# Kernel tuning notes

Measured on AMD Instinct MI355X. Metric: run time of the kernel, lower is better.

The kernel has to match this reference:

```python
import jax, jax.numpy as jnp
import numpy as np

VOCAB = 32
UTT_LEN = 16
NUM_MEANING_TYPES = 5
MEANINGS_PER_TYPE = 10
SUPPORT_SIZE = 100000  # = MEANINGS_PER_TYPE ** NUM_MEANING_TYPES
BATCH = 2048


def setup_inputs() -> dict:
    key = jax.random.key(0)
    k1, k2, k3 = jax.random.split(key, 3)
    # query utterances: [utt_len, batch] token ids
    utts = jax.random.randint(k1, (UTT_LEN, BATCH), 0, VOCAB, dtype=jnp.int64)
    # support set is stored as one-hot encoded utterances [S, utt_len*vocab]
    support_tokens = jax.random.randint(k2, (SUPPORT_SIZE, UTT_LEN), 0, VOCAB)
    support = jax.nn.one_hot(support_tokens, VOCAB, dtype=jnp.float32)
    support = support.reshape(SUPPORT_SIZE, UTT_LEN * VOCAB)
    # meanings table [S, num_meaning_types]
    meanings_t = jax.random.randint(k3, (SUPPORT_SIZE, NUM_MEANING_TYPES), 0,
                                    MEANINGS_PER_TYPE, dtype=jnp.int64)
    return {"utts": utts, "support": support, "meanings_t": meanings_t}


def reference(utts, support, meanings_t):
    # utts: [M, N] ints; support: [S, M*V] floats; meanings_t: [S, T] ints
    M, N = utts.shape
    # one-hot encode queries: [N, M, V] -> [N, M*V]
    batch_fluffy = jax.nn.one_hot(utts.T, VOCAB, dtype=jnp.float32).reshape(N, M * VOCAB)
    batch_sq = jnp.sum(batch_fluffy * batch_fluffy, axis=1)        # [N]
    support_sq = jnp.sum(support * support, axis=1)                # [S]
    cross = batch_fluffy @ support.T                                # [N, S]
    squared_dist = batch_sq[:, None] + support_sq[None, :] - 2.0 * cross
    # top-1 smallest distance (K=1)
    top1 = jnp.argmin(squared_dist, axis=1)                         # [N]
    meanings = meanings_t[top1]                                     # [N, T]
    return jax.nn.one_hot(meanings, MEANINGS_PER_TYPE, dtype=jnp.float32)
```

## Files before the change

kernel.cpp:

```cpp
#include <hip/hip_runtime.h>
#include <stdint.h>

#define S_ROWS 100000
#define NQ     2048
#define M_POS  16
#define VOCABS 32
#define NWORD  64
#define NBLK   250
#define RPB    400
#define RITER  16
#define KITER  25
#define TPB    1024

__device__ __forceinline__ void FA(uint32_t a, uint32_t b, uint32_t c,
                                   uint32_t& s, uint32_t& co) {
    uint32_t x = a ^ b;
    s  = x ^ c;
    co = (a & b) | (x & c);
}
__device__ __forceinline__ void HA(uint32_t a, uint32_t b, uint32_t& s, uint32_t& co) {
    s = a ^ b; co = a & b;
}

__device__ __forceinline__ void decode_row(float4 f0, float4 f1, int lane,
                                           uint8_t* __restrict__ dst) {
    float base = (float)((lane & 3) * 64);
    float v = f0.x * (base + 0.f)  + f0.y * (base + 8.f)  + f0.z * (base + 16.f) + f0.w * (base + 24.f)
            + f1.x * (base + 32.f) + f1.y * (base + 40.f) + f1.z * (base + 48.f) + f1.w * (base + 56.f);
    v += __shfl_xor(v, 1);
    v += __shfl_xor(v, 2);
    if ((lane & 3) == 0) dst[lane >> 2] = (uint8_t)(v + 0.5f);
}

__global__ __launch_bounds__(TPB, 4) void knn_fused(const int* __restrict__ utts,
                                                    const float* __restrict__ support,
                                                    uint32_t* __restrict__ best) {
    __shared__ uint32_t smem[M_POS * VOCABS * NWORD];
    __shared__ __align__(16) uint8_t tokbuf[2][RITER * 16];

    const int t    = threadIdx.x;
    const int c    = blockIdx.x;
    const int r0   = c * RPB;
    const int w    = t & 63;
    const int sub  = t >> 6;
    const int lane = t & 63;

    #pragma unroll
    for (int i = 0; i < 32; ++i) smem[t + 1024 * i] = 0u;
    __syncthreads();

    #pragma unroll
    for (int qq = 0; qq < 2; ++qq) {
        int q  = t + qq * 1024;
        int wb = q >> 5, j = q & 31;
        #pragma unroll
        for (int m = 0; m < M_POS; ++m) {
            int v = utts[m * NQ + q];
            atomicOr(&smem[(m * VOCABS + v) * NWORD + wb], 1u << j);
        }
    }

    const float4* gp = (const float4*)(support + (size_t)(r0 + sub) * 512) + lane * 2;
    float4 f0 = gp[0];
    float4 f1 = gp[1];
    gp += 2048;
    decode_row(f0, f1, lane, &tokbuf[0][sub * 16]);
    f0 = gp[0];
    f1 = gp[1];
    gp += 2048;
    __syncthreads();

    uint32_t cp0=0,cp1=0,cp2=0,cp3=0,cp4=0;
    uint32_t k0p=0,k1p=0,k2p=0,k3p=0,k4p=0;
    const uint32_t* tw = smem + w;

    #pragma unroll 5
    for (int i = 0; i < KITER; ++i) {
        uint4 ta = *(const uint4*)&tokbuf[i & 1][sub * 16];
        uint32_t b[16];
        b[0]  = tw[ (ta.x        & 0xFFu) * 8 +  0*2048];
        b[1]  = tw[((ta.x >> 8)  & 0xFFu) * 8 +  1*2048];
        b[2]  = tw[((ta.x >> 16) & 0xFFu) * 8 +  2*2048];
        b[3]  = tw[((ta.x >> 24)        ) * 8 +  3*2048];
        b[4]  = tw[ (ta.y        & 0xFFu) * 8 +  4*2048];
        b[5]  = tw[((ta.y >> 8)  & 0xFFu) * 8 +  5*2048];
        b[6]  = tw[((ta.y >> 16) & 0xFFu) * 8 +  6*2048];
        b[7]  = tw[((ta.y >> 24)        ) * 8 +  7*2048];
        b[8]  = tw[ (ta.z        & 0xFFu) * 8 +  8*2048];
        b[9]  = tw[((ta.z >> 8)  & 0xFFu) * 8 +  9*2048];
        b[10] = tw[((ta.z >> 16) & 0xFFu) * 8 + 10*2048];
        b[11] = tw[((ta.z >> 24)        ) * 8 + 11*2048];
        b[12] = tw[ (ta.w        & 0xFFu) * 8 + 12*2048];
        b[13] = tw[((ta.w >> 8)  & 0xFFu) * 8 + 13*2048];
        b[14] = tw[((ta.w >> 16) & 0xFFu) * 8 + 14*2048];
        b[15] = tw[((ta.w >> 24)        ) * 8 + 15*2048];

        uint32_t s10,s11,s12,s13,s14, c10,c11,c12,c13,c14;
        FA(b[0],b[1],b[2],   s10,c10);
        FA(b[3],b[4],b[5],   s11,c11);
        FA(b[6],b[7],b[8],   s12,c12);
        FA(b[9],b[10],b[11], s13,c13);
        FA(b[12],b[13],b[14],s14,c14);
        uint32_t s2a,c2a,s2b,c2b;
        FA(s10,s11,s12, s2a,c2a);
        FA(s13,s14,b[15], s2b,c2b);
        uint32_t n0,h0;  HA(s2a,s2b, n0,h0);
        uint32_t u,cu,vv,cv,x2,cx,n1,cy;
        FA(c10,c11,c12, u,cu);
        FA(c13,c14,c2a, vv,cv);
        FA(u,vv,c2b,    x2,cx);
        HA(x2,h0,       n1,cy);
        uint32_t y4,cz,n2,cw,n3,n4;
        FA(cu,cv,cx, y4,cz);
        HA(y4,cy,    n2,cw);
        HA(cz,cw,    n3,n4);

        uint32_t eq = ~(n4 ^ cp4);
        uint32_t gt = n4 & ~cp4;
        gt |= eq & (n3 & ~cp3);  eq &= ~(n3 ^ cp3);
        gt |= eq & (n2 & ~cp2);  eq &= ~(n2 ^ cp2);
        gt |= eq & (n1 & ~cp1);  eq &= ~(n1 ^ cp1);
        gt |= eq & (n0 & ~cp0);

        uint32_t ng = ~gt;
        cp0 = (gt & n0) | (ng & cp0);
        cp1 = (gt & n1) | (ng & cp1);
        cp2 = (gt & n2) | (ng & cp2);
        cp3 = (gt & n3) | (ng & cp3);
        cp4 = (gt & n4) | (ng & cp4);
        uint32_t kb0 = 0u - (uint32_t)( i       & 1);
        uint32_t kb1 = 0u - (uint32_t)((i >> 1) & 1);
        uint32_t kb2 = 0u - (uint32_t)((i >> 2) & 1);
        uint32_t kb3 = 0u - (uint32_t)((i >> 3) & 1);
        uint32_t kb4 = 0u - (uint32_t)((i >> 4) & 1);
        k0p = (k0p & ng) | (gt & kb0);
        k1p = (k1p & ng) | (gt & kb1);
        k2p = (k2p & ng) | (gt & kb2);
        k3p = (k3p & ng) | (gt & kb3);
        k4p = (k4p & ng) | (gt & kb4);

        if (i + 1 < KITER) {
            decode_row(f0, f1, lane, &tokbuf[(i + 1) & 1][sub * 16]);
            if (i + 2 < KITER) {
                f0 = gp[0];
                f1 = gp[1];
                gp += 2048;
            }
        }
        __syncthreads();
    }

    {
        uint32_t C  = 0x1FFFFu - (uint32_t)(r0 + sub);
        int       wp = (w + sub) & 63;
        #pragma unroll
        for (int j = 0; j < 32; ++j) {
            uint32_t cnt = ((cp0>>j)&1u) | (((cp1>>j)&1u)<<1) | (((cp2>>j)&1u)<<2)
                         | (((cp3>>j)&1u)<<3) | (((cp4>>j)&1u)<<4);
            uint32_t kk  = ((k0p>>j)&1u) | (((k1p>>j)&1u)<<1) | (((k2p>>j)&1u)<<2)
                         | (((k3p>>j)&1u)<<3) | (((k4p>>j)&1u)<<4);
            uint32_t key = (cnt << 17) + C - (kk << 4);
            smem[j * 1024 + sub * 64 + wp] = key;
        }
    }
    __syncthreads();

    {
        int w2 = t & 63;
        #pragma unroll
        for (int jj = 0; jj < 2; ++jj) {
            int j2 = (t >> 6) * 2 + jj;
            uint32_t bestv = 0;
            #pragma unroll
            for (int s = 0; s < 16; ++s) {
                uint32_t v = smem[j2 * 1024 + s * 64 + ((w2 + s) & 63)];
                bestv = bestv > v ? bestv : v;
            }
            atomicMax(&best[w2 * 32 + j2], bestv);
        }
    }
}

__global__ __launch_bounds__(256) void knn_out(const uint32_t* __restrict__ best,
                                               const int* __restrict__ meanings,
                                               float* __restrict__ out) {
    int q = blockIdx.x * 256 + threadIdx.x;
    if (q >= NQ) return;
    uint32_t b = best[q];
    int idx = 0x1FFFF - (int)(b & 0x1FFFFu);
    float* o = out + (size_t)q * 50;
    #pragma unroll
    for (int tt = 0; tt < 5; ++tt) {
        int mv = meanings[(size_t)idx * 5 + tt];
        #pragma unroll
        for (int mm = 0; mm < 10; ++mm) o[tt * 10 + mm] = (mm == mv) ? 1.0f : 0.0f;
    }
}

extern "C" void kernel_launch(void* const* d_in, const int* in_sizes, int n_in,
                              void* d_out, int out_size, void* d_ws, size_t ws_size,
                              hipStream_t stream) {
    const int*   utts     = (const int*)d_in[0];
    const float* support  = (const float*)d_in[1];
    const int*   meanings = (const int*)d_in[2];
    float* out = (float*)d_out;

    uint32_t* best = (uint32_t*)d_ws;

    hipMemsetAsync(best, 0, NQ * sizeof(uint32_t), stream);
    knn_fused<<<NBLK, TPB, 0, stream>>>(utts, support, best);
    knn_out<<<NQ / 256, 256, 0, stream>>>(best, meanings, out);
}
```

Before: 382.4 us.

## Broadcast decoded tokens via readlane and drop per-iteration block barriers

```diff
diff --git a/kernel.cpp b/kernel.cpp
--- a/kernel.cpp
+++ b/kernel.cpp
@@ -8,7 +8,6 @@
 #define NWORD  64
 #define NBLK   250
 #define RPB    400
-#define RITER  16
 #define KITER  25
 #define TPB    1024
 
@@ -22,21 +21,10 @@
     s = a ^ b; co = a & b;
 }
 
-__device__ __forceinline__ void decode_row(float4 f0, float4 f1, int lane,
-                                           uint8_t* __restrict__ dst) {
-    float base = (float)((lane & 3) * 64);
-    float v = f0.x * (base + 0.f)  + f0.y * (base + 8.f)  + f0.z * (base + 16.f) + f0.w * (base + 24.f)
-            + f1.x * (base + 32.f) + f1.y * (base + 40.f) + f1.z * (base + 48.f) + f1.w * (base + 56.f);
-    v += __shfl_xor(v, 1);
-    v += __shfl_xor(v, 2);
-    if ((lane & 3) == 0) dst[lane >> 2] = (uint8_t)(v + 0.5f);
-}
-
 __global__ __launch_bounds__(TPB, 4) void knn_fused(const int* __restrict__ utts,
                                                     const float* __restrict__ support,
                                                     uint32_t* __restrict__ best) {
     __shared__ uint32_t smem[M_POS * VOCABS * NWORD];
-    __shared__ __align__(16) uint8_t tokbuf[2][RITER * 16];
 
     const int t    = threadIdx.x;
     const int c    = blockIdx.x;
@@ -45,55 +33,58 @@
     const int sub  = t >> 6;
     const int lane = t & 63;
 
-    #pragma unroll
-    for (int i = 0; i < 32; ++i) smem[t + 1024 * i] = 0u;
-    __syncthreads();
-
-    #pragma unroll
-    for (int qq = 0; qq < 2; ++qq) {
-        int q  = t + qq * 1024;
-        int wb = q >> 5, j = q & 31;
+    {
+        const int m = sub;
+        uint32_t* col = smem + m * (VOCABS * NWORD) + w;
         #pragma unroll
-        for (int m = 0; m < M_POS; ++m) {
-            int v = utts[m * NQ + q];
-            atomicOr(&smem[(m * VOCABS + v) * NWORD + wb], 1u << j);
+        for (int v = 0; v < VOCABS; ++v) col[v * NWORD] = 0u;
+        const int4* qp = (const int4*)(utts + m * NQ + w * 32);
+        #pragma unroll
+        for (int jj = 0; jj < 8; ++jj) {
+            int4 q4 = qp[jj];
+            col[q4.x * NWORD] |= 1u << (jj * 4 + 0);
+            col[q4.y * NWORD] |= 1u << (jj * 4 + 1);
+            col[q4.z * NWORD] |= 1u << (jj * 4 + 2);
+            col[q4.w * NWORD] |= 1u << (jj * 4 + 3);
         }
     }
-
-    const float4* gp = (const float4*)(support + (size_t)(r0 + sub) * 512) + lane * 2;
-    float4 f0 = gp[0];
-    float4 f1 = gp[1];
-    gp += 2048;
-    decode_row(f0, f1, lane, &tokbuf[0][sub * 16]);
-    f0 = gp[0];
-    f1 = gp[1];
-    gp += 2048;
     __syncthreads();
 
     uint32_t cp0=0,cp1=0,cp2=0,cp3=0,cp4=0;
     uint32_t k0p=0,k1p=0,k2p=0,k3p=0,k4p=0;
-    const uint32_t* tw = smem + w;
 
-    #pragma unroll 5
+    const float4* gp = (const float4*)(support + (size_t)(r0 + sub) * 512) + lane * 2;
+    float4 f0  = gp[0];
+    float4 f1  = gp[1];
+    gp += 2048;
+    float4 f0n = gp[0];
+    float4 f1n = gp[1];
+    gp += 2048;
+
+    const int w4 = w << 2;
+
+    #pragma unroll 2
     for (int i = 0; i < KITER; ++i) {
-        uint4 ta = *(const uint4*)&tokbuf[i & 1][sub * 16];
+        float base = (float)((lane & 3) * 64);
+        float v = f0.x * (base + 0.f)  + f0.y * (base + 8.f)  + f0.z * (base + 16.f) + f0.w * (base + 24.f)
+                + f1.x * (base + 32.f) + f1.y * (base + 40.f) + f1.z * (base + 48.f) + f1.w * (base + 56.f);
+        v += __shfl_xor(v, 1);
+        v += __shfl_xor(v, 2);
+        int vi = (int)(v + 0.5f);
+
+        f0 = f0n; f1 = f1n;
+        if (i + 2 < KITER) {
+            f0n = gp[0];
+            f1n = gp[1];
+            gp += 2048;
+        }
+
         uint32_t b[16];
-        b[0]  = tw[ (ta.x        & 0xFFu) * 8 +  0*2048];
-        b[1]  = tw[((ta.x >> 8)  & 0xFFu) * 8 +  1*2048];
-        b[2]  = tw[((ta.x >> 16) & 0xFFu) * 8 +  2*2048];
-        b[3]  = tw[((ta.x >> 24)        ) * 8 +  3*2048];
-        b[4]  = tw[ (ta.y        & 0xFFu) * 8 +  4*2048];
-        b[5]  = tw[((ta.y >> 8)  & 0xFFu) * 8 +  5*2048];
-        b[6]  = tw[((ta.y >> 16) & 0xFFu) * 8 +  6*2048];
-        b[7]  = tw[((ta.y >> 24)        ) * 8 +  7*2048];
-        b[8]  = tw[ (ta.z        & 0xFFu) * 8 +  8*2048];
-        b[9]  = tw[((ta.z >> 8)  & 0xFFu) * 8 +  9*2048];
-        b[10] = tw[((ta.z >> 16) & 0xFFu) * 8 + 10*2048];
-        b[11] = tw[((ta.z >> 24)        ) * 8 + 11*2048];
-        b[12] = tw[ (ta.w        & 0xFFu) * 8 + 12*2048];
-        b[13] = tw[((ta.w >> 8)  & 0xFFu) * 8 + 13*2048];
-        b[14] = tw[((ta.w >> 16) & 0xFFu) * 8 + 14*2048];
-        b[15] = tw[((ta.w >> 24)        ) * 8 + 15*2048];
+        #pragma unroll
+        for (int m = 0; m < M_POS; ++m) {
+            int vm8 = __builtin_amdgcn_readlane(vi, 4 * m);
+            b[m] = *(const uint32_t*)((const char*)smem + (m * 8192 + vm8 * 32) + w4);
+        }
 
         uint32_t s10,s11,s12,s13,s14, c10,c11,c12,c13,c14;
         FA(b[0],b[1],b[2],   s10,c10);
@@ -138,17 +129,9 @@
         k2p = (k2p & ng) | (gt & kb2);
         k3p = (k3p & ng) | (gt & kb3);
         k4p = (k4p & ng) | (gt & kb4);
+    }
 
-        if (i + 1 < KITER) {
-            decode_row(f0, f1, lane, &tokbuf[(i + 1) & 1][sub * 16]);
-            if (i + 2 < KITER) {
-                f0 = gp[0];
-                f1 = gp[1];
-                gp += 2048;
-            }
-        }
-        __syncthreads();
-    }
+    __syncthreads();
 
     {
         uint32_t C  = 0x1FFFFu - (uint32_t)(r0 + sub);
```

Result: slower. 511.9 us (+33.9%).
